# Performance work log

Hardware: AMD Instinct MI355X
Metric: run time of the kernel (lower is better)

## Reference

```python
import jax, jax.numpy as jnp
import numpy as np

TOP_K = 2
EPS = 1e-9


def setup_inputs() -> dict:
    key = jax.random.key(0)
    k1, k2, k3, k4 = jax.random.split(key, 4)
    B, T, D, H, E = 4, 2048, 1024, 4096, 8
    x = jax.random.normal(k1, (B, T, D), dtype=jnp.float32)
    Wr = jax.random.normal(k2, (D, E), dtype=jnp.float32) * 0.02
    W1 = jax.random.normal(k3, (E, D, H), dtype=jnp.float32) * 0.02
    W2 = jax.random.normal(k4, (E, H, D), dtype=jnp.float32) * 0.02
    return {"x": x, "Wr": Wr, "W1": W1, "W2": W2}


def reference(x, Wr, W1, W2):
    # x: (B,T,D); Wr: (D,E); W1: (E,D,H); W2: (E,H,D)
    E = Wr.shape[1]
    logits = jnp.einsum('btd,de->bte', x, Wr)          # (B,T,E)
    probs = jax.nn.softmax(logits, axis=-1)
    top_p, top_i = jax.lax.top_k(probs, TOP_K)         # (B,T,K)
    gates = top_p / (jnp.sum(top_p, axis=-1, keepdims=True) + EPS)
    # combine weights per expert: (B,T,E), zero where expert not selected
    oh = jax.nn.one_hot(top_i, E, dtype=x.dtype)       # (B,T,K,E)
    comb = jnp.sum(oh * gates[..., None], axis=2)      # (B,T,E)
    out = jnp.zeros_like(x)
    for e in range(E):  # fixed small expert loop
        h = jax.nn.gelu(jnp.einsum('btd,dh->bth', x, W1[e]), approximate=False)
        y = jnp.einsum('bth,hd->btd', h, W2[e])
        out = out + comb[..., e:e + 1] * y
    # load-balancing loss (on detached stats, matching torch .detach())
    mask = (jnp.sum(oh, axis=2) > 0).astype(jnp.float32)  # (B,T,E)
    imp = jnp.sum(jax.lax.stop_gradient(probs), axis=(0, 1))
    load = jnp.sum(jax.lax.stop_gradient(mask), axis=(0, 1))
    imp = imp / (jnp.sum(imp) + EPS)
    load = load / (jnp.sum(load) + EPS)
    lb = jnp.sum(imp * load) * E
    return out, lb
```

## Files before the change

kernel.cpp:

```cpp
#include <hip/hip_runtime.h>
#include <hip/hip_bf16.h>
#include <math.h>

#define NTOK 8192
#define DDIM 1024
#define HDIM 4096
#define NEXP 8
#define HROWS (NTOK*2 + 256)
#define RBLK 512

typedef unsigned int u32;
typedef unsigned short u16;
typedef __bf16 bf16x8 __attribute__((ext_vector_type(8)));
typedef float f32x4 __attribute__((ext_vector_type(4)));
typedef u32 u32x4 __attribute__((ext_vector_type(4)));
typedef u16 u16x8 __attribute__((ext_vector_type(8)));
typedef u16 u16x4 __attribute__((ext_vector_type(4)));

__device__ __forceinline__ u16 f2bf(float f){
  u32 u = __builtin_bit_cast(u32, f);
  u32 r = (u + 0x7FFFu + ((u >> 16) & 1u)) >> 16;
  return (u16)r;
}
__device__ __forceinline__ float bf2f(u16 b){
  u32 u = ((u32)b) << 16;
  return __builtin_bit_cast(float, u);
}
__device__ __forceinline__ void gl_lds16(const void* g, void* l){
  __builtin_amdgcn_global_load_lds(
      (const __attribute__((address_space(1))) u32*)g,
      (__attribute__((address_space(3))) u32*)l, 16, 0, 0);
}
__device__ __forceinline__ float gelu_t(float v){
  float u = v * (0.7978845608f + 0.0356774081f * v * v);
  float e = __expf(2.0f * u);
  float t = 1.0f - 2.0f / (e + 1.0f);
  return 0.5f * v * (1.0f + t);
}

__global__ __launch_bounds__(256) void transpose_cvt(const float* __restrict__ in,
                                                     u16* __restrict__ out,
                                                     int R, int C){
  int e = blockIdx.z;
  const float* pin = in + (long)e * R * C;
  u16* pout = out + (long)e * R * C;
  __shared__ u16 tile[64][129];
  int c0 = blockIdx.x * 128, r0 = blockIdx.y * 64;
  int tid = threadIdx.x;
#pragma unroll
  for (int j = 0; j < 8; j++){
    int f = tid + 256 * j;
    int r = f >> 5, c4 = (f & 31) << 2;
    float4 v = *(const float4*)(pin + (long)(r0 + r) * C + c0 + c4);
    tile[r][c4]     = f2bf(v.x);
    tile[r][c4 + 1] = f2bf(v.y);
    tile[r][c4 + 2] = f2bf(v.z);
    tile[r][c4 + 3] = f2bf(v.w);
  }
  __syncthreads();
#pragma unroll
  for (int j = 0; j < 4; j++){
    int g = tid + 256 * j;
    int oc = g >> 3;
    int r8 = (g & 7) << 3;
    u16x8 o;
#pragma unroll
    for (int i = 0; i < 8; i++) o[i] = tile[r8 + i][oc];
    *(u16x8*)(pout + (long)(c0 + oc) * R + r0 + r8) = o;
  }
}

__global__ __launch_bounds__(1024) void route_kernel(const float* __restrict__ x,
                                                     const float* __restrict__ Wr,
                                                     u16* __restrict__ xb,
                                                     int4* __restrict__ meta,
                                                     float2* __restrict__ gates,
                                                     int* __restrict__ selrk,
                                                     int* __restrict__ blockhist,
                                                     float* __restrict__ impPart){
  const int wid = threadIdx.x >> 6;
  const int lane = threadIdx.x & 63;
  const int t = blockIdx.x * 16 + wid;
  const float* xr = x + (long)t * DDIM;
  u16* xbr = xb + (long)t * DDIM;
  float acc[NEXP] = {};
  for (int d0 = lane * 4; d0 < DDIM; d0 += 256){
    float4 xv = *(const float4*)(xr + d0);
    u16x4 xo;
    xo[0] = f2bf(xv.x); xo[1] = f2bf(xv.y); xo[2] = f2bf(xv.z); xo[3] = f2bf(xv.w);
    *(u16x4*)(xbr + d0) = xo;
    const float* w = Wr + d0 * NEXP;
#pragma unroll
    for (int q = 0; q < 4; q++){
      float xq = ((const float*)&xv)[q];
      float4 w0 = *(const float4*)(w + q * NEXP);
      float4 w1 = *(const float4*)(w + q * NEXP + 4);
      acc[0] += xq * w0.x; acc[1] += xq * w0.y; acc[2] += xq * w0.z; acc[3] += xq * w0.w;
      acc[4] += xq * w1.x; acc[5] += xq * w1.y; acc[6] += xq * w1.z; acc[7] += xq * w1.w;
    }
  }
#pragma unroll
  for (int e = 0; e < NEXP; e++){
#pragma unroll
    for (int off = 32; off; off >>= 1) acc[e] += __shfl_xor(acc[e], off, 64);
  }
  __shared__ int sel_s[32];
  __shared__ float p_s[16][NEXP];
  if (lane == 0){
    float mx = acc[0];
#pragma unroll
    for (int e = 1; e < NEXP; e++) mx = fmaxf(mx, acc[e]);
    float p[NEXP]; float s = 0.f;
#pragma unroll
    for (int e = 0; e < NEXP; e++){ p[e] = expf(acc[e] - mx); s += p[e]; }
    float inv = 1.f / s;
#pragma unroll
    for (int e = 0; e < NEXP; e++){ p[e] *= inv; p_s[wid][e] = p[e]; }
    int i0 = 0; float v0 = p[0];
#pragma unroll
    for (int e = 1; e < NEXP; e++) if (p[e] > v0){ v0 = p[e]; i0 = e; }
    int i1 = -1; float v1 = -1.f;
#pragma unroll
    for (int e = 0; e < NEXP; e++) if (e != i0 && p[e] > v1){ v1 = p[e]; i1 = e; }
    float gs = v0 + v1 + 1e-9f;
    meta[t] = make_int4(i0, i1, 0, 0);
    gates[t] = make_float2(v0 / gs, v1 / gs);
    sel_s[wid * 2] = i0;
    sel_s[wid * 2 + 1] = i1;
  }
  __syncthreads();
  const int tid = threadIdx.x;
  if (tid < 32){
    int e = sel_s[tid];
    int r = 0;
    for (int m = 0; m < tid; m++) r += (sel_s[m] == e) ? 1 : 0;
    selrk[blockIdx.x * 32 + tid] = (r << 3) | e;
  }
  if (tid < NEXP){
    int hcount = 0;
#pragma unroll
    for (int m = 0; m < 32; m++) hcount += (sel_s[m] == tid) ? 1 : 0;
    blockhist[blockIdx.x * NEXP + tid] = hcount;
    float s = 0.f;
#pragma unroll
    for (int w = 0; w < 16; w++) s += p_s[w][tid];
    impPart[blockIdx.x * NEXP + tid] = s;
  }
}

__global__ __launch_bounds__(512) void scan_kernel(int* __restrict__ blockhist,
                                                   const float* __restrict__ impPart,
                                                   int* __restrict__ cnt,
                                                   int* __restrict__ offs,
                                                   float* __restrict__ imp){
  const int e = threadIdx.x >> 6;
  const int lane = threadIdx.x & 63;
  const int base = lane * 8;
  int v[8]; int s = 0;
#pragma unroll
  for (int i = 0; i < 8; i++){
    int tmp = blockhist[(base + i) * NEXP + e];
    v[i] = s; s += tmp;
  }
  int inc = s;
#pragma unroll
  for (int off = 1; off < 64; off <<= 1){
    int o = __shfl_up(inc, off, 64);
    if (lane >= off) inc += o;
  }
  int excl = inc - s;
#pragma unroll
  for (int i = 0; i < 8; i++) blockhist[(base + i) * NEXP + e] = v[i] + excl;
  int tot = __shfl(inc, 63, 64);
  float fs = 0.f;
#pragma unroll
  for (int i = 0; i < 8; i++) fs += impPart[(base + i) * NEXP + e];
#pragma unroll
  for (int off = 32; off; off >>= 1) fs += __shfl_xor(fs, off, 64);
  __shared__ int cnt_s[NEXP];
  if (lane == 0){ cnt_s[e] = tot; cnt[e] = tot; imp[e] = fs; }
  __syncthreads();
  if (threadIdx.x == 0){
    int o = 0;
    for (int q = 0; q < NEXP; q++){ offs[q] = o; o += cnt_s[q]; }
  }
}

__global__ __launch_bounds__(256) void fill_kernel(const int* __restrict__ selrk,
                                                   const int* __restrict__ blockhist,
                                                   int* __restrict__ elist,
                                                   int4* __restrict__ meta){
  int m = blockIdx.x * 256 + threadIdx.x;
  int t = m >> 1, c = m & 1, b = m >> 5;
  int pk = selrk[m];
  int e = pk & 7, r = pk >> 3;
  int gslot = blockhist[b * NEXP + e] + r;
  elist[e * NTOK + gslot] = t;
  ((int*)meta)[t * 4 + 2 + c] = gslot;
}

template<int KD, int ND, int TG, bool GATHER, bool GELU>
__global__ __launch_bounds__(512, 4) void gemm_tb(const u16* __restrict__ Ag,
                                                  const u16* __restrict__ Bg,
                                                  u16* __restrict__ Cg,
                                                  const int* __restrict__ elist,
                                                  const int* __restrict__ cnt,
                                                  const int* __restrict__ offs){
  const int NDB = ND / 256;
  const int bid = blockIdx.x;
  const int e  = bid & 7;
  const int le = bid >> 3;
  const int tti = le % TG;
  const int db  = (le / TG) % NDB;
  const int tg  = le / (TG * NDB);
  const int tt  = tg * TG + tti;
  const int n_e = cnt[e];
  if (tt * 128 >= n_e) return;
  const int cb = db * 256;
  __shared__ __align__(16) u16 As[3][128 * 32];
  __shared__ __align__(16) u16 Bs[3][256 * 32];
  const int tid = threadIdx.x;
  const int sch = (((tid & 3) ^ ((tid >> 2) & 3) ^ ((tid >> 4) & 3)) << 3);
  const int row0 = offs[e] + tt * 128;
  long agb;
  {
    int row = tid >> 2;
    int arow;
    if (GATHER){
      int slot = tt * 128 + row;
      if (slot >= n_e) slot = n_e - 1;
      arow = elist[e * NTOK + slot];
    } else {
      arow = row0 + row;
    }
    agb = (long)arow * KD + sch;
  }
  const long bbase = ((long)e * ND + cb) * KD;
  const long bgb0 = bbase + (long)(tid >> 2) * KD + sch;
  const long bgb1 = bbase + (long)(128 + (tid >> 2)) * KD + sch;
  const int ldst = tid * 8;

  const int l = tid & 63;
  const int w = tid >> 6;
  const int wm = w >> 2, wn = w & 3;
  const int fr = l & 15, fq = l >> 4;
  const int swz = ((fq ^ (fr & 3) ^ ((fr >> 2) & 3)) << 4);
  const u32 aB0 = (u32)(uintptr_t)&As[0][0] + (u32)((wm * 64 + fr) * 64 + swz);
  const u32 bB0 = (u32)(uintptr_t)&Bs[0][0] + (u32)((wn * 64 + fr) * 64 + swz);

  f32x4 acc[4][4] = {};
  const int NK = KD / 32;

#define STG(cbuf, kel) \
    gl_lds16(Ag + agb + (kel), &As[cbuf][ldst]); \
    gl_lds16(Bg + bgb0 + (kel), &Bs[cbuf][ldst]); \
    gl_lds16(Bg + bgb1 + (kel), &Bs[cbuf][4096 + ldst]);

  STG(0, 0)
  STG(1, 32)
  asm volatile("s_waitcnt vmcnt(3)" ::: "memory");
  __builtin_amdgcn_s_barrier();

  int c = 0;
  for (int k = 0; k < NK; ++k){
    const u32 aA = aB0 + (u32)(c * 8192);
    const u32 bA = bB0 + (u32)(c * 16384);
    u32x4 a[4], b[4];
    asm volatile("ds_read_b128 %0, %1"             : "=v"(b[0]) : "v"(bA));
    asm volatile("ds_read_b128 %0, %1 offset:1024" : "=v"(b[1]) : "v"(bA));
    asm volatile("ds_read_b128 %0, %1 offset:2048" : "=v"(b[2]) : "v"(bA));
    asm volatile("ds_read_b128 %0, %1 offset:3072" : "=v"(b[3]) : "v"(bA));
    asm volatile("ds_read_b128 %0, %1"             : "=v"(a[0]) : "v"(aA));
    asm volatile("ds_read_b128 %0, %1 offset:1024" : "=v"(a[1]) : "v"(aA));
    asm volatile("ds_read_b128 %0, %1 offset:2048" : "=v"(a[2]) : "v"(aA));
    asm volatile("ds_read_b128 %0, %1 offset:3072" : "=v"(a[3]) : "v"(aA));
    if (k + 2 < NK){
      int cn = c + 2; if (cn >= 3) cn -= 3;
      STG(cn, (k + 2) * 32)
    }
    asm volatile("s_waitcnt lgkmcnt(3)" ::: "memory");
    __builtin_amdgcn_sched_barrier(0);
#pragma unroll
    for (int n = 0; n < 4; n++)
      acc[0][n] = __builtin_amdgcn_mfma_f32_16x16x32_bf16(
          __builtin_bit_cast(bf16x8, a[0]), __builtin_bit_cast(bf16x8, b[n]),
          acc[0][n], 0, 0, 0);
    asm volatile("s_waitcnt lgkmcnt(2)" ::: "memory");
    __builtin_amdgcn_sched_barrier(0);
#pragma unroll
    for (int n = 0; n < 4; n++)
      acc[1][n] = __builtin_amdgcn_mfma_f32_16x16x32_bf16(
          __builtin_bit_cast(bf16x8, a[1]), __builtin_bit_cast(bf16x8, b[n]),
          acc[1][n], 0, 0, 0);
    asm volatile("s_waitcnt lgkmcnt(1)" ::: "memory");
    __builtin_amdgcn_sched_barrier(0);
#pragma unroll
    for (int n = 0; n < 4; n++)
      acc[2][n] = __builtin_amdgcn_mfma_f32_16x16x32_bf16(
          __builtin_bit_cast(bf16x8, a[2]), __builtin_bit_cast(bf16x8, b[n]),
          acc[2][n], 0, 0, 0);
    asm volatile("s_waitcnt lgkmcnt(0)" ::: "memory");
    __builtin_amdgcn_sched_barrier(0);
#pragma unroll
    for (int n = 0; n < 4; n++)
      acc[3][n] = __builtin_amdgcn_mfma_f32_16x16x32_bf16(
          __builtin_bit_cast(bf16x8, a[3]), __builtin_bit_cast(bf16x8, b[n]),
          acc[3][n], 0, 0, 0);
    if (k + 2 < NK){
      asm volatile("s_waitcnt vmcnt(3)" ::: "memory");
    } else if (k + 1 < NK){
      asm volatile("s_waitcnt vmcnt(0)" ::: "memory");
    }
    if (k + 1 < NK) __builtin_amdgcn_s_barrier();
    c += 1; if (c >= 3) c -= 3;
  }
#undef STG

#pragma unroll
  for (int m = 0; m < 4; m++){
#pragma unroll
    for (int j = 0; j < 4; j++){
      int row = wm * 64 + m * 16 + fq * 4 + j;
      int slot = tt * 128 + row;
      if (slot >= n_e) continue;
      long base = (long)(row0 + row) * ND + cb + wn * 64;
#pragma unroll
      for (int n = 0; n < 4; n++){
        float v = acc[m][n][j];
        if (GELU) v = gelu_t(v);
        Cg[base + n * 16 + fr] = f2bf(v);
      }
    }
  }
}

__global__ __launch_bounds__(256) void combine_kernel(const u16* __restrict__ ypair,
                                                      const int4* __restrict__ meta,
                                                      const float2* __restrict__ gates,
                                                      const int* __restrict__ offs,
                                                      float* __restrict__ out){
  int t = blockIdx.x;
  int c = threadIdx.x;
  int4 m = meta[t];
  float2 g = gates[t];
  long p0 = (long)(offs[m.x] + m.z) * DDIM + c * 4;
  long p1 = (long)(offs[m.y] + m.w) * DDIM + c * 4;
  u16x4 y0 = *(const u16x4*)&ypair[p0];
  u16x4 y1 = *(const u16x4*)&ypair[p1];
  float4 o;
  o.x = g.x * bf2f(y0[0]) + g.y * bf2f(y1[0]);
  o.y = g.x * bf2f(y0[1]) + g.y * bf2f(y1[1]);
  o.z = g.x * bf2f(y0[2]) + g.y * bf2f(y1[2]);
  o.w = g.x * bf2f(y0[3]) + g.y * bf2f(y1[3]);
  *(float4*)&out[(long)t * DDIM + c * 4] = o;
}

__global__ void lb_kernel(const float* __restrict__ imp, const int* __restrict__ cnt,
                          float* __restrict__ outp){
  if (threadIdx.x == 0 && blockIdx.x == 0){
    float si = 0.f, sl = 0.f;
    for (int e = 0; e < NEXP; e++){ si += imp[e]; sl += (float)cnt[e]; }
    float lb = 0.f;
    for (int e = 0; e < NEXP; e++)
      lb += (imp[e] / (si + 1e-9f)) * ((float)cnt[e] / (sl + 1e-9f));
    outp[0] = lb * (float)NEXP;
  }
}

extern "C" void kernel_launch(void* const* d_in, const int* in_sizes, int n_in,
                              void* d_out, int out_size, void* d_ws, size_t ws_size,
                              hipStream_t stream){
  const float* x  = (const float*)d_in[0];
  const float* Wr = (const float*)d_in[1];
  const float* W1 = (const float*)d_in[2];
  const float* W2 = (const float*)d_in[3];
  float* out = (float*)d_out;
  char* ws = (char*)d_ws;
  size_t off = 0;
  u16* xb = (u16*)(ws + off);   off += (size_t)NTOK * DDIM * 2;
  u16* wt = (u16*)(ws + off);   off += (size_t)NEXP * DDIM * HDIM * 2;
  u16* h  = (u16*)(ws + off);   off += (size_t)HROWS * HDIM * 2;
  u16* yp = (u16*)(ws + off);   off += (size_t)NTOK * 2 * DDIM * 2;
  int* elist    = (int*)(ws + off);    off += (size_t)NEXP * NTOK * 4;
  int4* meta    = (int4*)(ws + off);   off += (size_t)NTOK * 16;
  float2* gts   = (float2*)(ws + off); off += (size_t)NTOK * 8;
  int* selrk    = (int*)(ws + off);    off += (size_t)NTOK * 2 * 4;
  int* bhist    = (int*)(ws + off);    off += (size_t)RBLK * NEXP * 4;
  float* impP   = (float*)(ws + off);  off += (size_t)RBLK * NEXP * 4;
  int* cnt      = (int*)(ws + off);    off += 32;
  float* imp    = (float*)(ws + off);  off += 32;
  int* offs     = (int*)(ws + off);    off += 32;
  if (ws_size < off) return;

  route_kernel<<<RBLK, 1024, 0, stream>>>(x, Wr, xb, meta, gts, selrk, bhist, impP);
  scan_kernel<<<1, 512, 0, stream>>>(bhist, impP, cnt, offs, imp);
  fill_kernel<<<NTOK * 2 / 256, 256, 0, stream>>>(selrk, bhist, elist, meta);
  transpose_cvt<<<dim3(HDIM / 128, DDIM / 64, NEXP), 256, 0, stream>>>(W1, wt, DDIM, HDIM);
  gemm_tb<DDIM, HDIM, 8, true, true><<<NEXP * 64 * (HDIM / 256), 512, 0, stream>>>(
      xb, wt, h, elist, cnt, offs);
  transpose_cvt<<<dim3(DDIM / 128, HDIM / 64, NEXP), 256, 0, stream>>>(W2, wt, HDIM, DDIM);
  gemm_tb<HDIM, DDIM, 2, false, false><<<NEXP * 64 * (DDIM / 256), 512, 0, stream>>>(
      h, wt, yp, elist, cnt, offs);
  combine_kernel<<<NTOK, 256, 0, stream>>>(yp, meta, gts, offs, out);
  lb_kernel<<<1, 64, 0, stream>>>(imp, cnt, out + (size_t)NTOK * DDIM);
}
```

Measured before the change: 516.2 us.

## Fuse gated combine into second expert GEMM epilogue with atomic adds

The second grouped GEMM now scatters its gate-scaled fp32 accumulators straight into the output with atomicAdd, using the token index from elist and a per-slot gate written by fill_kernel. This removes the bf16 ypair intermediate buffer and the separate combine kernel, but the output must now be zeroed with a memset first. The epilogue pays for this with scattered fp32 atomics (two contributions per element) and a nondeterministic summation order.

```diff
diff --git a/kernel.cpp b/kernel.cpp
--- a/kernel.cpp
+++ b/kernel.cpp
@@ -188,7 +188,9 @@
 
 __global__ __launch_bounds__(256) void fill_kernel(const int* __restrict__ selrk,
                                                    const int* __restrict__ blockhist,
+                                                   const float2* __restrict__ gates,
                                                    int* __restrict__ elist,
+                                                   float* __restrict__ agate,
                                                    int4* __restrict__ meta){
   int m = blockIdx.x * 256 + threadIdx.x;
   int t = m >> 1, c = m & 1, b = m >> 5;
@@ -196,6 +198,8 @@
   int e = pk & 7, r = pk >> 3;
   int gslot = blockhist[b * NEXP + e] + r;
   elist[e * NTOK + gslot] = t;
+  float2 g = gates[t];
+  agate[e * NTOK + gslot] = c ? g.y : g.x;
   ((int*)meta)[t * 4 + 2 + c] = gslot;
 }
 
@@ -203,6 +207,8 @@
 __global__ __launch_bounds__(512, 4) void gemm_tb(const u16* __restrict__ Ag,
                                                   const u16* __restrict__ Bg,
                                                   u16* __restrict__ Cg,
+                                                  float* __restrict__ outp,
+                                                  const float* __restrict__ agate,
                                                   const int* __restrict__ elist,
                                                   const int* __restrict__ cnt,
                                                   const int* __restrict__ offs){
@@ -323,36 +329,21 @@
       int row = wm * 64 + m * 16 + fq * 4 + j;
       int slot = tt * 128 + row;
       if (slot >= n_e) continue;
-      long base = (long)(row0 + row) * ND + cb + wn * 64;
-#pragma unroll
-      for (int n = 0; n < 4; n++){
-        float v = acc[m][n][j];
-        if (GELU) v = gelu_t(v);
-        Cg[base + n * 16 + fr] = f2bf(v);
+      if (GELU){
+        long base = (long)(row0 + row) * ND + cb + wn * 64;
+#pragma unroll
+        for (int n = 0; n < 4; n++)
+          Cg[base + n * 16 + fr] = f2bf(gelu_t(acc[m][n][j]));
+      } else {
+        int tok = elist[e * NTOK + slot];
+        float g = agate[e * NTOK + slot];
+        long base = (long)tok * ND + cb + wn * 64;
+#pragma unroll
+        for (int n = 0; n < 4; n++)
+          atomicAdd(&outp[base + n * 16 + fr], g * acc[m][n][j]);
       }
     }
   }
-}
-
-__global__ __launch_bounds__(256) void combine_kernel(const u16* __restrict__ ypair,
-                                                      const int4* __restrict__ meta,
-                                                      const float2* __restrict__ gates,
-                                                      const int* __restrict__ offs,
-                                                      float* __restrict__ out){
-  int t = blockIdx.x;
-  int c = threadIdx.x;
-  int4 m = meta[t];
-  float2 g = gates[t];
-  long p0 = (long)(offs[m.x] + m.z) * DDIM + c * 4;
-  long p1 = (long)(offs[m.y] + m.w) * DDIM + c * 4;
-  u16x4 y0 = *(const u16x4*)&ypair[p0];
-  u16x4 y1 = *(const u16x4*)&ypair[p1];
-  float4 o;
-  o.x = g.x * bf2f(y0[0]) + g.y * bf2f(y1[0]);
-  o.y = g.x * bf2f(y0[1]) + g.y * bf2f(y1[1]);
-  o.z = g.x * bf2f(y0[2]) + g.y * bf2f(y1[2]);
-  o.w = g.x * bf2f(y0[3]) + g.y * bf2f(y1[3]);
-  *(float4*)&out[(long)t * DDIM + c * 4] = o;
 }
 
 __global__ void lb_kernel(const float* __restrict__ imp, const int* __restrict__ cnt,
@@ -380,8 +371,8 @@
   u16* xb = (u16*)(ws + off);   off += (size_t)NTOK * DDIM * 2;
   u16* wt = (u16*)(ws + off);   off += (size_t)NEXP * DDIM * HDIM * 2;
   u16* h  = (u16*)(ws + off);   off += (size_t)HROWS * HDIM * 2;
-  u16* yp = (u16*)(ws + off);   off += (size_t)NTOK * 2 * DDIM * 2;
   int* elist    = (int*)(ws + off);    off += (size_t)NEXP * NTOK * 4;
+  float* agate  = (float*)(ws + off);  off += (size_t)NEXP * NTOK * 4;
   int4* meta    = (int4*)(ws + off);   off += (size_t)NTOK * 16;
   float2* gts   = (float2*)(ws + off); off += (size_t)NTOK * 8;
   int* selrk    = (int*)(ws + off);    off += (size_t)NTOK * 2 * 4;
@@ -392,15 +383,15 @@
   int* offs     = (int*)(ws + off);    off += 32;
   if (ws_size < off) return;
 
+  hipMemsetAsync(out, 0, (size_t)NTOK * DDIM * 4, stream);
   route_kernel<<<RBLK, 1024, 0, stream>>>(x, Wr, xb, meta, gts, selrk, bhist, impP);
   scan_kernel<<<1, 512, 0, stream>>>(bhist, impP, cnt, offs, imp);
-  fill_kernel<<<NTOK * 2 / 256, 256, 0, stream>>>(selrk, bhist, elist, meta);
+  fill_kernel<<<NTOK * 2 / 256, 256, 0, stream>>>(selrk, bhist, gts, elist, agate, meta);
   transpose_cvt<<<dim3(HDIM / 128, DDIM / 64, NEXP), 256, 0, stream>>>(W1, wt, DDIM, HDIM);
   gemm_tb<DDIM, HDIM, 8, true, true><<<NEXP * 64 * (HDIM / 256), 512, 0, stream>>>(
-      xb, wt, h, elist, cnt, offs);
+      xb, wt, h, nullptr, nullptr, elist, cnt, offs);
   transpose_cvt<<<dim3(DDIM / 128, HDIM / 64, NEXP), 256, 0, stream>>>(W2, wt, HDIM, DDIM);
   gemm_tb<HDIM, DDIM, 2, false, false><<<NEXP * 64 * (DDIM / 256), 512, 0, stream>>>(
-      h, wt, yp, elist, cnt, offs);
-  combine_kernel<<<NTOK, 256, 0, stream>>>(yp, meta, gts, offs, out);
+      h, wt, nullptr, out, agate, elist, cnt, offs);
   lb_kernel<<<1, 64, 0, stream>>>(imp, cnt, out + (size_t)NTOK * DDIM);
 }
```

Measured after the change: 545.6 us. 1.06x slower.
